# Optimization experiments

Measured on AMD Instinct MI355X. Metric: run time of the kernel, lower is better.

The kernel has to match this reference:

```python
import jax, jax.numpy as jnp
import numpy as np

TLEN, BSZ, HID = 64, 32, 1024
SLEN = 200
V_TGT = 32000
V_EXT = 2000
UNK = 0  # ext_dict UNK index, ignored in the onehot scatter


def setup_inputs() -> dict:
    key = jax.random.key(0)
    ks = jax.random.split(key, 6)
    hidden = jax.random.normal(ks[0], (TLEN, BSZ, HID), dtype=jnp.float32)
    attn = jax.random.uniform(ks[1], (TLEN, BSZ, SLEN), dtype=jnp.float32)
    attn = attn / jnp.sum(attn, axis=-1, keepdims=True)  # attention-like distribution
    copy_to_ext = jax.random.randint(ks[2], (SLEN, BSZ), 0, V_EXT)
    W_out = jax.random.normal(ks[3], (V_TGT, HID), dtype=jnp.float32) * 0.02
    b_out = jnp.zeros((V_TGT,), dtype=jnp.float32)
    w_copy = jax.random.normal(ks[4], (1, HID), dtype=jnp.float32) * 0.02
    b_copy = jnp.zeros((1,), dtype=jnp.float32)
    return {"hidden": hidden, "attn": attn, "copy_to_ext": copy_to_ext,
            "W_out": W_out, "b_out": b_out, "w_copy": w_copy, "b_copy": b_copy}


def _safe_log(v):
    return jnp.log(jnp.clip(v, 0.001, 1.0 - 0.001))


def reference(hidden, attn, copy_to_ext, W_out, b_out, w_copy, b_copy):
    tlen, bsz, hid = hidden.shape
    slen = attn.shape[-1]
    h = hidden.reshape(tlen * bsz, hid)
    a = attn.reshape(tlen * bsz, slen)

    # p(copy) gate
    copy = jax.nn.sigmoid(h @ w_copy.T + b_copy)            # [N, 1]
    # generator log-probs over tgt vocab
    logits = h @ W_out.T + b_out                            # [N, V_TGT]
    prob_log = jax.nn.log_softmax(logits, axis=-1)
    out_prob_log = prob_log + _safe_log(copy)

    # attention mass scaled by (1 - p(copy)) -- NOTE: matches source exactly
    mul_attn = a * (1.0 - copy)                             # [N, SLEN]
    mul_attn_b = mul_attn.reshape(tlen, bsz, slen).transpose(1, 0, 2)  # [B, T, S]
    idx = copy_to_ext.T                                     # [B, S]

    def per_batch(m, i):
        # m: [T, S], i: [S]; scatter-add attn mass into ext vocab, ignoring UNK
        valid = (i != UNK).astype(m.dtype)                  # onehot ignore_index
        return jax.ops.segment_sum((m * valid).T, i, num_segments=V_EXT).T  # [T, E]

    ext_copy_prob = jax.vmap(per_batch)(mul_attn_b, idx)    # [B, T, E]
    ext_copy_prob = ext_copy_prob.transpose(1, 0, 2).reshape(tlen * bsz, V_EXT)
    ext_copy_prob_log = _safe_log(ext_copy_prob)

    out = jnp.concatenate([out_prob_log, ext_copy_prob_log], axis=1)
    return out.reshape(tlen, bsz, V_TGT + V_EXT)
```

## Files before the change

### kernel.cpp

```cpp
#include <hip/hip_runtime.h>
#include <cstdint>
#include <cstddef>

#define TLEN 64
#define BSZ  32
#define NROW 2048
#define HID  1024
#define SLEN 200
#define VT   32000
#define VE   2000
#define OUTW 34000

#define BM 256
#define BN 256
#define BK 64
#define NMT 8
#define NNT 125
#define NBN 125

typedef float  f32x4  __attribute__((ext_vector_type(4)));
typedef __bf16 bf16x4 __attribute__((ext_vector_type(4)));
typedef __bf16 bf16x8 __attribute__((ext_vector_type(8)));
typedef float  floatx4 __attribute__((ext_vector_type(4)));

__global__ __launch_bounds__(256) void prep_kernel(
    const float* __restrict__ h, const float* __restrict__ wc,
    const float* __restrict__ bc, const float* __restrict__ W,
    __bf16* __restrict__ Hbf, __bf16* __restrict__ Wbf,
    float* __restrict__ logcopy, float* __restrict__ oneminus) {
  int tid = threadIdx.x;
  if (blockIdx.x < NROW) {
    int row = blockIdx.x;
    f32x4 v  = ((const f32x4*)(h + (size_t)row * HID))[tid];
    f32x4 wv = ((const f32x4*)wc)[tid];
    bf16x4 o;
    o.x = (__bf16)v.x; o.y = (__bf16)v.y; o.z = (__bf16)v.z; o.w = (__bf16)v.w;
    ((bf16x4*)(Hbf + (size_t)row * HID))[tid] = o;
    float s = v.x * wv.x + v.y * wv.y + v.z * wv.z + v.w * wv.w;
    #pragma unroll
    for (int off = 32; off; off >>= 1) s += __shfl_down(s, off, 64);
    __shared__ float wsum[4];
    int lane = tid & 63, w = tid >> 6;
    if (lane == 0) wsum[w] = s;
    __syncthreads();
    if (tid == 0) {
      float x = wsum[0] + wsum[1] + wsum[2] + wsum[3] + bc[0];
      float pc = 1.f / (1.f + __expf(-x));
      float pcc = fminf(fmaxf(pc, 0.001f), 0.999f);
      logcopy[row]  = logf(pcc);
      oneminus[row] = 1.f - pc;
    }
  } else {
    const int n4 = (VT * HID) / 4;
    int i = (blockIdx.x - NROW) * 256 + tid;
    for (; i < n4; i += 4096 * 256) {
      f32x4 v = __builtin_nontemporal_load(((const f32x4*)W) + i);
      bf16x4 o;
      o.x = (__bf16)v.x; o.y = (__bf16)v.y; o.z = (__bf16)v.z; o.w = (__bf16)v.w;
      ((bf16x4*)Wbf)[i] = o;
    }
  }
}


__device__ __forceinline__ void load_lds16(const __bf16* g, __bf16* s) {
  __builtin_amdgcn_global_load_lds(
      (const __attribute__((address_space(1))) void*)g,
      (__attribute__((address_space(3))) void*)s, 16, 0, 0);
}

__device__ __forceinline__ void loadB4(const __bf16* Sb, int offB, int ga,
                                       bf16x8 bfr[4]) {
  #pragma unroll
  for (int j = 0; j < 4; j++)
    bfr[j] = *(const bf16x8*)(Sb + offB + j * 1024 + ga);
}

template<int RG>
__device__ __forceinline__ void loadA4(const __bf16* Sa, int offA, int ga,
                                       bf16x8 af[4]) {
  #pragma unroll
  for (int i = 0; i < 4; i++)
    af[i] = *(const bf16x8*)(Sa + offA + (RG * 4 + i) * 1024 + ga);
}

template<int RG>
__device__ __forceinline__ void mfma16(floatx4 (&acc)[8][4], const bf16x8 af[4],
                                       const bf16x8 bfr[4]) {
  __builtin_amdgcn_s_setprio(1);
  #pragma unroll
  for (int i = 0; i < 4; i++)
    #pragma unroll
    for (int j = 0; j < 4; j++)
      acc[RG * 4 + i][j] =
          __builtin_amdgcn_mfma_f32_16x16x32_bf16(af[i], bfr[j],
                                                  acc[RG * 4 + i][j], 0, 0, 0);
  __builtin_amdgcn_s_setprio(0);
}

#define VM2 asm volatile("s_waitcnt vmcnt(2)" ::: "memory")
#define VM0 asm volatile("s_waitcnt vmcnt(0)" ::: "memory")

__global__ __launch_bounds__(512) void gemm_kernel(
    const __bf16* __restrict__ A, const __bf16* __restrict__ B,
    const float* __restrict__ bias, float* __restrict__ out) {
  __shared__ __attribute__((aligned(16))) __bf16 Asb[2][BM * BK];
  __shared__ __attribute__((aligned(16))) __bf16 Bsb[2][BN * BK];

  const int tid = threadIdx.x;
  const int swz = ((int)blockIdx.x & 7) * 125 + ((int)blockIdx.x >> 3);
  const int bm = swz & 7;
  const int bn = swz >> 3;

  const int r0s = tid >> 3,         g0 = tid & 7;
  const int r1s = (512 + tid) >> 3, g1 = (512 + tid) & 7;
  const int gs0 = (g0 ^ (r0s & 7)) * 8;
  const int gs1 = (g1 ^ (r1s & 7)) * 8;

  const __bf16* Abase = A + (size_t)bm * BM * HID;
  const __bf16* Bbase = B + (size_t)bn * BN * HID;

  const int l = tid & 63, w = tid >> 6;
  const int wm = w & 1;
  const int wn = w >> 1;
  const int lr = l & 15, q = l >> 4;
  const int x7 = lr & 7;
  const int offA = (wm * 128 + lr) * 64;
  const int offB = (wn * 64 + lr) * 64;
  const int ga0 = (q ^ x7) * 8;
  const int ga1 = ((4 + q) ^ x7) * 8;

#define STAGE_A(dst, h, kt) do { \
    load_lds16(Abase + (size_t)((h) * 128 + r0s) * HID + (kt) * 64 + gs0, \
               (dst) + (h) * 8192 + tid * 8); \
    load_lds16(Abase + (size_t)((h) * 128 + r1s) * HID + (kt) * 64 + gs1, \
               (dst) + (h) * 8192 + 4096 + tid * 8); \
  } while (0)
#define STAGE_B(dst, h, kt) do { \
    load_lds16(Bbase + (size_t)((h) * 128 + r0s) * HID + (kt) * 64 + gs0, \
               (dst) + (h) * 8192 + tid * 8); \
    load_lds16(Bbase + (size_t)((h) * 128 + r1s) * HID + (kt) * 64 + gs1, \
               (dst) + (h) * 8192 + 4096 + tid * 8); \
  } while (0)

  bf16x8 af[4], bfr[4];
  floatx4 acc[8][4] = {};

#define TILE_BLOCK(CA, CB, SA, SB, stk, DOST, VMASM) do {                    \
                                                       \
    if (DOST) STAGE_A(SA, 0, stk);                                           \
    VMASM;                                                                   \
    __builtin_amdgcn_s_barrier();                                            \
    loadB4(CB, offB, ga0, bfr);                                              \
    loadA4<0>(CA, offA, ga0, af);                                            \
    mfma16<0>(acc, af, bfr);                                                 \
    __builtin_amdgcn_s_barrier();                                            \
                                                       \
    loadA4<1>(CA, offA, ga0, af);                                            \
    if (DOST) STAGE_A(SA, 1, stk);                                           \
    __builtin_amdgcn_s_barrier();                                            \
    mfma16<1>(acc, af, bfr);                                                 \
    __builtin_amdgcn_s_barrier();                                            \
                                                       \
    loadB4(CB, offB, ga1, bfr);                                              \
    loadA4<0>(CA, offA, ga1, af);                                            \
    if (DOST) STAGE_B(SB, 0, stk);                                           \
    __builtin_amdgcn_s_barrier();                                            \
    mfma16<0>(acc, af, bfr);                                                 \
    __builtin_amdgcn_s_barrier();                                            \
                                                       \
    loadA4<1>(CA, offA, ga1, af);                                            \
    if (DOST) STAGE_B(SB, 1, stk);                                           \
    __builtin_amdgcn_s_barrier();                                            \
    mfma16<1>(acc, af, bfr);                                                 \
    __builtin_amdgcn_s_barrier();                                            \
  } while (0)

  STAGE_A(Asb[0], 0, 0); STAGE_A(Asb[0], 1, 0);
  STAGE_B(Bsb[0], 0, 0); STAGE_B(Bsb[0], 1, 0);

  for (int i = 0; i < 7; i++) {
    TILE_BLOCK(Asb[0], Bsb[0], Asb[1], Bsb[1], 2 * i + 1, true, VM2);
    TILE_BLOCK(Asb[1], Bsb[1], Asb[0], Bsb[0], 2 * i + 2, true, VM2);
  }
  TILE_BLOCK(Asb[0], Bsb[0], Asb[1], Bsb[1], 15, true, VM2);
  TILE_BLOCK(Asb[1], Bsb[1], Asb[0], Bsb[0], 0, false, VM0);

  __syncthreads();
  float* lS = (float*)Asb;

  const int col0 = bn * BN + wn * 64 + lr;
  const int row0 = bm * BM + wm * 128 + q * 4;
  float bv[4];
  #pragma unroll
  for (int j = 0; j < 4; j++) bv[j] = bias[col0 + j * 16];

  #pragma unroll
  for (int fi = 0; fi < 8; fi++) {
    #pragma unroll
    for (int r = 0; r < 4; r++) {
      int m = row0 + fi * 16 + r;
      float* po = out + (size_t)m * OUTW + col0;
      float vj[4];
      #pragma unroll
      for (int j = 0; j < 4; j++) vj[j] = acc[fi][j][r] + bv[j];
      #pragma unroll
      for (int j = 0; j < 4; j++) po[j * 16] = vj[j];
      float s4 = __expf(vj[0]) + __expf(vj[1]) + __expf(vj[2]) + __expf(vj[3]);
      #pragma unroll
      for (int off = 1; off < 16; off <<= 1) s4 += __shfl_xor(s4, off, 64);
      if (lr == 0) lS[wn * BM + wm * 128 + fi * 16 + q * 4 + r] = s4;
    }
  }
  __syncthreads();
  if (tid < BM) {
    float S = lS[tid] + lS[BM + tid] + lS[2 * BM + tid] + lS[3 * BM + tid];
    out[(size_t)(bm * BM + tid) * OUTW + VT + bn] = S;
  }
#undef TILE_BLOCK
#undef STAGE_A
#undef STAGE_B
}

__global__ __launch_bounds__(256) void finish_kernel(
    const float* __restrict__ attn, const int* __restrict__ c2e,
    const float* __restrict__ logcopy, const float* __restrict__ oneminus,
    float* __restrict__ out) {
  __shared__ float ext[VE];
  __shared__ float rS[4];
  int row = blockIdx.x;
  int tid = threadIdx.x;
  int b = row & (BSZ - 1);
  float* orow = out + (size_t)row * OUTW;

  float S = (tid < NBN) ? orow[VT + tid] : 0.f;

  for (int e = tid; e < VE; e += 256) ext[e] = 0.f;

  #pragma unroll
  for (int off = 32; off; off >>= 1) S += __shfl_down(S, off, 64);
  int lane = tid & 63, w = tid >> 6;
  if (lane == 0) rS[w] = S;
  __syncthreads();
  float sub = logf(rS[0] + rS[1] + rS[2] + rS[3]) - logcopy[row];

  float om1 = oneminus[row];
  if (tid < SLEN) {
    int idx = c2e[tid * BSZ + b];
    if (idx != 0)
      atomicAdd(&ext[idx], attn[(size_t)row * SLEN + tid] * om1);
  }

  #pragma unroll 4
  for (int k2 = 0; k2 < 31; k2++) {
    f32x4* p = (f32x4*)orow + (tid + k2 * 256);
    f32x4 v = *p;
    v = v - sub;
    __builtin_nontemporal_store(v, p);
  }
  {
    float v = orow[31744 + tid];
    __builtin_nontemporal_store(v - sub, orow + 31744 + tid);
  }

  __syncthreads();
  for (int e = tid; e < VE; e += 256)
    __builtin_nontemporal_store(logf(fminf(fmaxf(ext[e], 0.001f), 0.999f)),
                                orow + VT + e);
}

extern "C" void kernel_launch(void* const* d_in, const int* in_sizes, int n_in,
                              void* d_out, int out_size, void* d_ws, size_t ws_size,
                              hipStream_t stream) {
  const float* hidden = (const float*)d_in[0];
  const float* attn   = (const float*)d_in[1];
  const int*   c2e    = (const int*)d_in[2];
  const float* W      = (const float*)d_in[3];
  const float* bout   = (const float*)d_in[4];
  const float* wc     = (const float*)d_in[5];
  const float* bc     = (const float*)d_in[6];
  float* out = (float*)d_out;

  char* ws = (char*)d_ws;
  __bf16* Hbf = (__bf16*)ws;
  __bf16* Wbf = (__bf16*)(ws + 4194304);
  float* logcopy  = (float*)(ws + 4194304 + 65536000);
  float* oneminus = logcopy + NROW;

  prep_kernel<<<NROW + 4096, 256, 0, stream>>>(hidden, wc, bc, W, Hbf, Wbf,
                                               logcopy, oneminus);
  gemm_kernel<<<NMT * NNT, 512, 0, stream>>>(Hbf, Wbf, bout, out);
  finish_kernel<<<NROW, 256, 0, stream>>>(attn, c2e, logcopy, oneminus, out);
}
```

Measured before the change: 590.1 us.

## Stream B operands directly from global into registers, stage only A in LDS

Restructures the GEMM main loop so only the A tile is staged in LDS, in 128-wide K chunks with double buffering. Each wave reads its B fragments straight from global memory into registers. The goal is fewer barriers per K step and less LDS traffic and footprint. In exchange, B global loads are uncoalesced 16-byte per-lane reads with no LDS reuse across the two wm waves, and a full vmcnt(0) wait per chunk may expose latency.

```diff
diff --git a/kernel.cpp b/kernel.cpp
--- a/kernel.cpp
+++ b/kernel.cpp
@@ -13,7 +13,7 @@
 
 #define BM 256
 #define BN 256
-#define BK 64
+#define CHK 128
 #define NMT 8
 #define NNT 125
 #define NBN 125
@@ -69,122 +69,79 @@
       (__attribute__((address_space(3))) void*)s, 16, 0, 0);
 }
 
-__device__ __forceinline__ void loadB4(const __bf16* Sb, int offB, int ga,
-                                       bf16x8 bfr[4]) {
-  #pragma unroll
-  for (int j = 0; j < 4; j++)
-    bfr[j] = *(const bf16x8*)(Sb + offB + j * 1024 + ga);
-}
-
-template<int RG>
-__device__ __forceinline__ void loadA4(const __bf16* Sa, int offA, int ga,
-                                       bf16x8 af[4]) {
-  #pragma unroll
-  for (int i = 0; i < 4; i++)
-    af[i] = *(const bf16x8*)(Sa + offA + (RG * 4 + i) * 1024 + ga);
-}
-
-template<int RG>
-__device__ __forceinline__ void mfma16(floatx4 (&acc)[8][4], const bf16x8 af[4],
-                                       const bf16x8 bfr[4]) {
-  __builtin_amdgcn_s_setprio(1);
-  #pragma unroll
-  for (int i = 0; i < 4; i++)
-    #pragma unroll
-    for (int j = 0; j < 4; j++)
-      acc[RG * 4 + i][j] =
-          __builtin_amdgcn_mfma_f32_16x16x32_bf16(af[i], bfr[j],
-                                                  acc[RG * 4 + i][j], 0, 0, 0);
-  __builtin_amdgcn_s_setprio(0);
-}
-
-#define VM2 asm volatile("s_waitcnt vmcnt(2)" ::: "memory")
-#define VM0 asm volatile("s_waitcnt vmcnt(0)" ::: "memory")
-
 __global__ __launch_bounds__(512) void gemm_kernel(
     const __bf16* __restrict__ A, const __bf16* __restrict__ B,
     const float* __restrict__ bias, float* __restrict__ out) {
-  __shared__ __attribute__((aligned(16))) __bf16 Asb[2][BM * BK];
-  __shared__ __attribute__((aligned(16))) __bf16 Bsb[2][BN * BK];
+  __shared__ __attribute__((aligned(16))) __bf16 Asb[2][BM * CHK];
 
   const int tid = threadIdx.x;
   const int swz = ((int)blockIdx.x & 7) * 125 + ((int)blockIdx.x >> 3);
   const int bm = swz & 7;
   const int bn = swz >> 3;
 
-  const int r0s = tid >> 3,         g0 = tid & 7;
-  const int r1s = (512 + tid) >> 3, g1 = (512 + tid) & 7;
-  const int gs0 = (g0 ^ (r0s & 7)) * 8;
-  const int gs1 = (g1 ^ (r1s & 7)) * 8;
-
-  const __bf16* Abase = A + (size_t)bm * BM * HID;
-  const __bf16* Bbase = B + (size_t)bn * BN * HID;
+  const int g15 = tid & 15;
+  const int sg = (g15 & 8) | ((g15 ^ ((tid >> 4) & 7)) & 7);
+  const __bf16* asrc = A + (size_t)(bm * BM + (tid >> 4)) * HID + sg * 8;
+  __bf16* adst0 = &Asb[0][tid * 8];
+  __bf16* adst1 = &Asb[1][tid * 8];
+
+#define STAGE8(dst, ktn) do {                                              \
+    _Pragma("unroll")                                                      \
+    for (int i_ = 0; i_ < 8; i_++)                                         \
+      load_lds16(asrc + i_ * 32 * HID + (ktn), (dst) + i_ * 4096);         \
+  } while (0)
 
   const int l = tid & 63, w = tid >> 6;
   const int wm = w & 1;
   const int wn = w >> 1;
   const int lr = l & 15, q = l >> 4;
   const int x7 = lr & 7;
-  const int offA = (wm * 128 + lr) * 64;
-  const int offB = (wn * 64 + lr) * 64;
-  const int ga0 = (q ^ x7) * 8;
-  const int ga1 = ((4 + q) ^ x7) * 8;
-
-#define STAGE_A(dst, h, kt) do { \
-    load_lds16(Abase + (size_t)((h) * 128 + r0s) * HID + (kt) * 64 + gs0, \
-               (dst) + (h) * 8192 + tid * 8); \
-    load_lds16(Abase + (size_t)((h) * 128 + r1s) * HID + (kt) * 64 + gs1, \
-               (dst) + (h) * 8192 + 4096 + tid * 8); \
+  const int aoffr = (wm * 128 + lr) * CHK;
+  int gaK[4];
+  #pragma unroll
+  for (int ks = 0; ks < 4; ks++) {
+    int lg = ks * 4 + q;
+    gaK[ks] = ((lg & 8) | ((lg ^ x7) & 7)) * 8;
+  }
+  const __bf16* bp = B + (size_t)(bn * BN + wn * 64 + lr) * HID + q * 8;
+
+  floatx4 acc[8][4] = {};
+
+#define CHUNK(CUR, NXT, KTB, KTN, DOST) do {                               \
+    const __bf16* Ar = (CUR) + aoffr;                                      \
+    _Pragma("unroll")                                                      \
+    for (int ks = 0; ks < 4; ks++) {                                       \
+      bf16x8 bf[4], af[8];                                                 \
+      _Pragma("unroll")                                                    \
+      for (int j = 0; j < 4; j++)                                          \
+        bf[j] = *(const bf16x8*)(bp + (KTB) + ks * 32 + j * 16 * HID);     \
+      _Pragma("unroll")                                                    \
+      for (int i = 0; i < 8; i++)                                          \
+        af[i] = *(const bf16x8*)(Ar + i * 16 * CHK + gaK[ks]);             \
+      if (ks == 0 && (DOST)) STAGE8(NXT, KTN);                             \
+      _Pragma("unroll")                                                    \
+      for (int i = 0; i < 8; i++)                                          \
+        _Pragma("unroll")                                                  \
+        for (int j = 0; j < 4; j++)                                        \
+          acc[i][j] = __builtin_amdgcn_mfma_f32_16x16x32_bf16(             \
+              af[i], bf[j], acc[i][j], 0, 0, 0);                           \
+    }                                                                      \
+    asm volatile("s_waitcnt vmcnt(0)" ::: "memory");                       \
+    __builtin_amdgcn_s_barrier();                                          \
   } while (0)
-#define STAGE_B(dst, h, kt) do { \
-    load_lds16(Bbase + (size_t)((h) * 128 + r0s) * HID + (kt) * 64 + gs0, \
-               (dst) + (h) * 8192 + tid * 8); \
-    load_lds16(Bbase + (size_t)((h) * 128 + r1s) * HID + (kt) * 64 + gs1, \
-               (dst) + (h) * 8192 + 4096 + tid * 8); \
-  } while (0)
-
-  bf16x8 af[4], bfr[4];
-  floatx4 acc[8][4] = {};
-
-#define TILE_BLOCK(CA, CB, SA, SB, stk, DOST, VMASM) do {                    \
-                                                       \
-    if (DOST) STAGE_A(SA, 0, stk);                                           \
-    VMASM;                                                                   \
-    __builtin_amdgcn_s_barrier();                                            \
-    loadB4(CB, offB, ga0, bfr);                                              \
-    loadA4<0>(CA, offA, ga0, af);                                            \
-    mfma16<0>(acc, af, bfr);                                                 \
-    __builtin_amdgcn_s_barrier();                                            \
-                                                       \
-    loadA4<1>(CA, offA, ga0, af);                                            \
-    if (DOST) STAGE_A(SA, 1, stk);                                           \
-    __builtin_amdgcn_s_barrier();                                            \
-    mfma16<1>(acc, af, bfr);                                                 \
-    __builtin_amdgcn_s_barrier();                                            \
-                                                       \
-    loadB4(CB, offB, ga1, bfr);                                              \
-    loadA4<0>(CA, offA, ga1, af);                                            \
-    if (DOST) STAGE_B(SB, 0, stk);                                           \
-    __builtin_amdgcn_s_barrier();                                            \
-    mfma16<0>(acc, af, bfr);                                                 \
-    __builtin_amdgcn_s_barrier();                                            \
-                                                       \
-    loadA4<1>(CA, offA, ga1, af);                                            \
-    if (DOST) STAGE_B(SB, 1, stk);                                           \
-    __builtin_amdgcn_s_barrier();                                            \
-    mfma16<1>(acc, af, bfr);                                                 \
-    __builtin_amdgcn_s_barrier();                                            \
-  } while (0)
-
-  STAGE_A(Asb[0], 0, 0); STAGE_A(Asb[0], 1, 0);
-  STAGE_B(Bsb[0], 0, 0); STAGE_B(Bsb[0], 1, 0);
-
-  for (int i = 0; i < 7; i++) {
-    TILE_BLOCK(Asb[0], Bsb[0], Asb[1], Bsb[1], 2 * i + 1, true, VM2);
-    TILE_BLOCK(Asb[1], Bsb[1], Asb[0], Bsb[0], 2 * i + 2, true, VM2);
-  }
-  TILE_BLOCK(Asb[0], Bsb[0], Asb[1], Bsb[1], 15, true, VM2);
-  TILE_BLOCK(Asb[1], Bsb[1], Asb[0], Bsb[0], 0, false, VM0);
+
+  STAGE8(adst0, 0);
+  asm volatile("s_waitcnt vmcnt(0)" ::: "memory");
+  __builtin_amdgcn_s_barrier();
+
+  CHUNK(Asb[0], adst1, 0,   128, true);
+  CHUNK(Asb[1], adst0, 128, 256, true);
+  CHUNK(Asb[0], adst1, 256, 384, true);
+  CHUNK(Asb[1], adst0, 384, 512, true);
+  CHUNK(Asb[0], adst1, 512, 640, true);
+  CHUNK(Asb[1], adst0, 640, 768, true);
+  CHUNK(Asb[0], adst1, 768, 896, true);
+  CHUNK(Asb[1], adst0, 896, 0,   false);
 
   __syncthreads();
   float* lS = (float*)Asb;
@@ -217,9 +174,8 @@
     float S = lS[tid] + lS[BM + tid] + lS[2 * BM + tid] + lS[3 * BM + tid];
     out[(size_t)(bm * BM + tid) * OUTW + VT + bn] = S;
   }
-#undef TILE_BLOCK
-#undef STAGE_A
-#undef STAGE_B
+#undef CHUNK
+#undef STAGE8
 }
 
 __global__ __launch_bounds__(256) void finish_kernel(
```

After: 630.0 us. 1.07x slower.
